# Kernel optimization log

Measured on AMD Instinct MI355X. Metric: run time of the kernel, lower is better.

## Reference

```python
import jax, jax.numpy as jnp
import numpy as np

B, SC, ST = 16, 512, 512
DP, DC = 256, 128
D = DP + 2 * DC          # 512 = d_model
H, L, DFF = 8, 2, 2048
NCAT, NCONT = 1000, 2048


def sin_embed(vals, d, scale=1000.0):
    # vectorized sinusoidal_time_embedding: even dims -> sin(angle), odd dims -> cos(angle)
    i = jnp.arange(d, dtype=jnp.float32)
    ang = vals.astype(jnp.float32)[..., None] / jnp.power(scale, i / d)
    return jnp.where(i % 2 == 0, jnp.sin(ang), jnp.cos(ang))


def layer_norm(x, g, b, eps=1e-5):
    m = jnp.mean(x, -1, keepdims=True)
    v = jnp.mean(jnp.square(x - m), -1, keepdims=True)
    return (x - m) / jnp.sqrt(v + eps) * g + b


def setup_inputs() -> dict:
    key = jax.random.key(0)
    ks = jax.random.split(key, 16)
    s = 0.02
    def n(k, shape, scale=s):
        return jax.random.normal(k, shape, dtype=jnp.float32) * scale
    return {
        "context_cat": jax.random.randint(ks[0], (B, SC), 0, NCAT),
        "context_time": jax.random.uniform(ks[1], (B, SC), dtype=jnp.float32) * 100.0,
        "context_f0": jax.random.uniform(ks[2], (B, SC), dtype=jnp.float32) * 500.0,
        "target_cat": jax.random.randint(ks[3], (B, ST), 0, NCAT),
        "target_time": jax.random.uniform(ks[4], (B, ST), dtype=jnp.float32) * 100.0,
        "target_f0": jax.random.uniform(ks[5], (B, ST), dtype=jnp.float32) * 500.0,
        "cat_table": n(ks[6], (NCAT, DP), 1.0),
        "cont_table": sin_embed(jnp.arange(NCONT, dtype=jnp.float32), DC),  # frozen sin table
        "pad_emb": n(ks[7], (D,), 1.0),
        "Wq": n(ks[8], (L, D, D)), "bq": jnp.zeros((L, D)),
        "Wk": n(ks[9], (L, D, D)), "bk": jnp.zeros((L, D)),
        "Wv": n(ks[10], (L, D, D)), "bv": jnp.zeros((L, D)),
        "Wo": n(ks[11], (L, D, D)), "bo": jnp.zeros((L, D)),
        "ln1g": jnp.ones((L, D)), "ln1b": jnp.zeros((L, D)),
        "ln2g": jnp.ones((L, D)), "ln2b": jnp.zeros((L, D)),
        "W1": n(ks[12], (L, D, DFF)), "b1": jnp.zeros((L, DFF)),
        "W2": n(ks[13], (L, DFF, D)), "b2": jnp.zeros((L, D)),
    }


def reference(context_cat, context_time, context_f0, target_cat, target_time, target_f0,
              cat_table, cont_table, pad_emb,
              Wq, bq, Wk, bk, Wv, bv, Wo, bo,
              ln1g, ln1b, ln2g, ln2b, W1, b1, W2, b2):
    def embed(cat, tm, f0):
        pad = cat < 0
        e = jnp.concatenate(
            [cat_table[jnp.maximum(cat, 0)], sin_embed(tm, DC), sin_embed(f0, DC)], axis=-1)
        return jnp.where(pad[..., None], pad_emb, e), pad

    ce, cp = embed(context_cat, context_time, context_f0)
    te, tp = embed(target_cat, target_time, target_f0)
    x = jnp.concatenate([ce, te], axis=1)                       # [B, SC+ST, D]
    bias = jnp.where(jnp.concatenate([cp, tp], 1), -1e9, 0.0)[:, None, None, :]
    hd = D // H
    inv_sqrt = 1.0 / np.sqrt(hd).astype(np.float32)

    def step(h, p):
        wq, bq_, wk, bk_, wv, bv_, wo, bo_, g1, c1, g2, c2, w1, d1, w2, d2 = p
        Bn, S, _ = h.shape
        q = (h @ wq + bq_).reshape(Bn, S, H, hd)
        k = (h @ wk + bk_).reshape(Bn, S, H, hd)
        v = (h @ wv + bv_).reshape(Bn, S, H, hd)
        scores = jnp.einsum('bqhd,bkhd->bhqk', q, k) * inv_sqrt + bias
        attn = jax.nn.softmax(scores, axis=-1)
        o = jnp.einsum('bhqk,bkhd->bqhd', attn, v).reshape(Bn, S, D)
        h = layer_norm(h + o @ wo + bo_, g1, c1)                # post-norm (torch default)
        f = jax.nn.relu(h @ w1 + d1) @ w2 + d2
        return layer_norm(h + f, g2, c2), None

    x, _ = jax.lax.scan(step, x, (Wq, bq, Wk, bk, Wv, bv, Wo, bo,
                                  ln1g, ln1b, ln2g, ln2b, W1, b1, W2, b2))
    out = x[:, SC:, :]
    pred_cat = out[..., :DP] @ cat_table.T
    pred_time = out[..., DP:DP + DC] @ cont_table.T
    pred_f0 = out[..., DP + DC:] @ cont_table.T
    return pred_cat, pred_time, pred_f0
```

## Files before the change

kernel.cpp:

```cpp
#include <hip/hip_runtime.h>


typedef _Float16 half8 __attribute__((ext_vector_type(8)));
typedef _Float16 half4 __attribute__((ext_vector_type(4)));
typedef float f32x4 __attribute__((ext_vector_type(4)));
typedef unsigned int uint2v __attribute__((ext_vector_type(2)));
typedef unsigned int uint4v __attribute__((ext_vector_type(4)));

__device__ __forceinline__ void gl2lds16(const _Float16* g, _Float16* l) {
    __builtin_amdgcn_global_load_lds(
        (const __attribute__((address_space(1))) void*)g,
        (__attribute__((address_space(3))) void*)l, 16, 0, 0);
}

__global__ void cast_f32_f16_k(const float* __restrict__ in, _Float16* __restrict__ out,
                               long nsrc, long ntot) {
    long i = (long)blockIdx.x * blockDim.x + threadIdx.x;
    long stride = (long)gridDim.x * blockDim.x;
    for (; i < ntot; i += stride) out[i] = i < nsrc ? (_Float16)in[i] : (_Float16)0.f;
}

__global__ void tcast_k(const float* __restrict__ in, _Float16* __restrict__ out,
                        int R, int C, long zs, int rowoff) {
    __shared__ float tile[32][33];
    long z = blockIdx.z;
    const float* src = in + z * (long)R * C;
    _Float16* dst = out + z * zs + (long)rowoff * R;
    int c0 = blockIdx.x * 32, r0 = blockIdx.y * 32;
    for (int i = threadIdx.y; i < 32; i += 8)
        tile[i][threadIdx.x] = src[(long)(r0 + i) * C + c0 + threadIdx.x];
    __syncthreads();
    for (int i = threadIdx.y; i < 32; i += 8)
        dst[(long)(c0 + i) * R + r0 + threadIdx.x] = (_Float16)tile[threadIdx.x][i];
}

__global__ void bcat_k(const float* __restrict__ bq, const float* __restrict__ bk,
                       const float* __restrict__ bv, float* __restrict__ out, int L) {
    int i = blockIdx.x * 256 + threadIdx.x;
    if (i >= L * 1536) return;
    int l = i / 1536, j = i - l * 1536;
    float v = j < 512 ? bq[l * 512 + j] : (j < 1024 ? bk[l * 512 + j - 512] : bv[l * 512 + j - 1024]);
    out[i] = v;
}

__global__ void vtrans_k(const _Float16* __restrict__ qkv, _Float16* __restrict__ vT) {
    __shared__ _Float16 tile[32][33];
    int bh = blockIdx.z; int b = bh >> 3, h = bh & 7;
    int s0 = blockIdx.x * 32, d0 = blockIdx.y * 32;
    const _Float16* src = qkv + ((long)b * 1024) * 1536 + 1024 + h * 64;
    _Float16* dst = vT + (long)bh * 64 * 1024;
    for (int i = threadIdx.y; i < 32; i += 8)
        tile[i][threadIdx.x] = src[(long)(s0 + i) * 1536 + d0 + threadIdx.x];
    __syncthreads();
    for (int i = threadIdx.y; i < 32; i += 8)
        dst[(long)(d0 + i) * 1024 + s0 + threadIdx.x] = tile[threadIdx.x][i];
}

__global__ __launch_bounds__(128) void embed_k(
    const int* __restrict__ ccat, const float* __restrict__ ctime, const float* __restrict__ cf0,
    const int* __restrict__ tcat, const float* __restrict__ ttime, const float* __restrict__ tf0,
    const float* __restrict__ cat_table, const float* __restrict__ pad_emb,
    float* __restrict__ xf, _Float16* __restrict__ xb, float* __restrict__ biasKey) {
    int t = blockIdx.x;
    int b = t >> 10, s = t & 1023;
    int j = b * 512 + (s & 511);
    int cat; float tm, f0;
    if (s < 512) { cat = ccat[j]; tm = ctime[j]; f0 = cf0[j]; }
    else         { cat = tcat[j]; tm = ttime[j]; f0 = tf0[j]; }
    bool pad = cat < 0;
    if (threadIdx.x == 0) biasKey[t] = pad ? -1e9f : 0.f;
    int c = cat < 0 ? 0 : cat;
    #pragma unroll
    for (int u = 0; u < 4; u++) {
        int d = threadIdx.x * 4 + u;
        float val;
        if (pad) val = pad_emb[d];
        else if (d < 256) val = cat_table[(long)c * 256 + d];
        else {
            float base = (d < 384) ? tm : f0;
            int i = (d < 384) ? (d - 256) : (d - 384);
            float ang = base / powf(1000.f, (float)i * (1.f / 128.f));
            val = (i & 1) ? cosf(ang) : sinf(ang);
        }
        long o = (long)t * 512 + d;
        xf[o] = val;
        xb[o] = (_Float16)val;
    }
}

__global__ __launch_bounds__(256) void layernorm_k(
    float* xf, _Float16* __restrict__ xb,
    const float* __restrict__ g, const float* __restrict__ beta) {
    long row = blockIdx.x;
    int tid = threadIdx.x;
    float* xr = xf + row * 512;
    float v0 = xr[tid], v1 = xr[tid + 256];
    float s = v0 + v1, q = v0 * v0 + v1 * v1;
    #pragma unroll
    for (int o = 32; o; o >>= 1) { s += __shfl_down(s, o); q += __shfl_down(q, o); }
    __shared__ float rs[4], rq[4];
    if ((tid & 63) == 0) { rs[tid >> 6] = s; rq[tid >> 6] = q; }
    __syncthreads();
    s = rs[0] + rs[1] + rs[2] + rs[3];
    q = rq[0] + rq[1] + rq[2] + rq[3];
    float mean = s * (1.f / 512.f);
    float var = q * (1.f / 512.f) - mean * mean;
    float rstd = rsqrtf(var + 1e-5f);
    float y0 = (v0 - mean) * rstd * g[tid] + beta[tid];
    float y1 = (v1 - mean) * rstd * g[tid + 256] + beta[tid + 256];
    xr[tid] = y0; xr[tid + 256] = y1;
    xb[row * 512 + tid] = (_Float16)y0;
    xb[row * 512 + tid + 256] = (_Float16)y1;
}

__global__ __launch_bounds__(512, 2) void flash_k(
    const _Float16* __restrict__ QKV, const _Float16* __restrict__ VT,
    const float* __restrict__ biasKey, _Float16* __restrict__ O) {
    const int S = 1024, D = 512, LDQ = 1536, NT = 16;
    int bh = blockIdx.x; int b = bh >> 3, h = bh & 7;
    int qt = blockIdx.y;
    int tid = threadIdx.x, w = tid >> 6, lane = tid & 63;
    int g = lane >> 4, q15 = lane & 15;

    __shared__ __align__(16) _Float16 Ks[2][64 * 64];
    __shared__ __align__(16) _Float16 VTs[2][64 * 64];
    __shared__ __align__(16) float biasLds[1024];

    {
        const float* bsrc = biasKey + (long)b * S;
        biasLds[tid]       = bsrc[tid] * 1.442695041f;
        biasLds[tid + 512] = bsrc[tid + 512] * 1.442695041f;
    }

    int qrow = qt * 128 + w * 16 + q15;
    const _Float16* qp = QKV + ((long)(b * S + qrow)) * LDQ + h * 64 + g * 8;
    half8 qf[2];
    qf[0] = *(const half8*)(qp);
    qf[1] = *(const half8*)(qp + 32);
    const _Float16 qsc = (_Float16)0.1803368801f;
    #pragma unroll
    for (int kk = 0; kk < 2; kk++)
        #pragma unroll
        for (int i = 0; i < 8; i++) qf[kk][i] *= qsc;

    const _Float16* kbase = QKV + 512 + ((long)b * S) * LDQ + h * 64;
    const _Float16* vbase = VT + (long)bh * 64 * S;

    auto stageK = [&](int buf, int kt) {
        int row = tid >> 3, p = tid & 7;
        int s = p ^ (row & 7);
        gl2lds16(kbase + (long)(kt * 64 + row) * LDQ + s * 8, &Ks[buf][tid * 8]);
    };
    auto stageV = [&](int buf, int kt) {
        int row = tid >> 3, p = tid & 7;
        int s = p ^ (row & 7);
        gl2lds16(vbase + (long)row * S + kt * 64 + s * 8, &VTs[buf][tid * 8]);
    };

    f32x4 acc_o[4];
    #pragma unroll
    for (int i = 0; i < 4; i++)
        #pragma unroll
        for (int r = 0; r < 4; r++) acc_o[i][r] = 0.f;
    float m_run = -1e30f, l_run = 0.f;
    bool gOdd = (g & 1) != 0;

    auto QK = [&](int kt, f32x4 (&s)[4]) {
        #pragma unroll
        for (int mf = 0; mf < 4; mf++)
            #pragma unroll
            for (int r = 0; r < 4; r++) s[mf][r] = 0.f;
        int buf = kt & 1;
        __builtin_amdgcn_s_setprio(1);
        #pragma unroll
        for (int kk = 0; kk < 2; kk++)
            #pragma unroll
            for (int mf = 0; mf < 4; mf++) {
                int row = mf * 16 + q15;
                half8 kf = *(const half8*)&Ks[buf][row * 64 + (((kk * 4 + g) ^ (row & 7)) * 8)];
                s[mf] = __builtin_amdgcn_mfma_f32_16x16x32_f16(kf, qf[kk], s[mf], 0, 0, 0);
            }
        __builtin_amdgcn_s_setprio(0);
    };

    auto SMPV = [&](int kt, f32x4 (&s)[4]) {
        float mt = -1e30f;
        #pragma unroll
        for (int mf = 0; mf < 4; mf++) {
            f32x4 b4 = *(const f32x4*)&biasLds[kt * 64 + mf * 16 + g * 4];
            #pragma unroll
            for (int r = 0; r < 4; r++) {
                float sv = s[mf][r] + b4[r];
                s[mf][r] = sv;
                mt = fmaxf(mt, sv);
            }
        }
        mt = fmaxf(mt, __shfl_xor(mt, 16));
        mt = fmaxf(mt, __shfl_xor(mt, 32));

        float rsum = 0.f;
        if (__all(mt - m_run <= 8.f)) {
            #pragma unroll
            for (int mf = 0; mf < 4; mf++)
                #pragma unroll
                for (int r = 0; r < 4; r++) {
                    float p = exp2f(s[mf][r] - m_run);
                    s[mf][r] = p; rsum += p;
                }
        } else {
            float m_new = fmaxf(m_run, mt);
            float scale = exp2f(m_run - m_new);
            #pragma unroll
            for (int mf = 0; mf < 4; mf++)
                #pragma unroll
                for (int r = 0; r < 4; r++) {
                    float p = exp2f(s[mf][r] - m_new);
                    s[mf][r] = p; rsum += p;
                }
            float sc[4];
            #pragma unroll
            for (int r = 0; r < 4; r++) sc[r] = __shfl(scale, g * 4 + r);
            #pragma unroll
            for (int nf = 0; nf < 4; nf++)
                #pragma unroll
                for (int r = 0; r < 4; r++) acc_o[nf][r] *= sc[r];
            l_run *= scale;
            m_run = m_new;
        }
        rsum += __shfl_xor(rsum, 16);
        rsum += __shfl_xor(rsum, 32);
        l_run += rsum;

        unsigned pk[4][2];
        #pragma unroll
        for (int mf = 0; mf < 4; mf++) {
            auto h0 = __builtin_amdgcn_cvt_pkrtz(s[mf][0], s[mf][1]);
            auto h1 = __builtin_amdgcn_cvt_pkrtz(s[mf][2], s[mf][3]);
            pk[mf][0] = __builtin_bit_cast(unsigned, h0);
            pk[mf][1] = __builtin_bit_cast(unsigned, h1);
        }

        int buf = kt & 1;
        #pragma unroll
        for (int kk = 0; kk < 2; kk++) {
            unsigned wA[2], wB[2];
            #pragma unroll
            for (int wi = 0; wi < 2; wi++) {
                uint2v r2 = __builtin_amdgcn_permlane32_swap(
                    pk[2 * kk][wi], pk[2 * kk + 1][wi], false, false);
                unsigned na = r2[0];
                unsigned nb = r2[1];
                unsigned sa = (unsigned)__builtin_amdgcn_ds_swizzle((int)na, 0x401F);
                unsigned sb = (unsigned)__builtin_amdgcn_ds_swizzle((int)nb, 0x401F);
                wA[wi] = gOdd ? sb : na;
                wB[wi] = gOdd ? nb : sa;
            }
            uint4v paw;
            paw[0] = wA[0]; paw[1] = wA[1]; paw[2] = wB[0]; paw[3] = wB[1];
            half8 pa = __builtin_bit_cast(half8, paw);
            __builtin_amdgcn_s_setprio(1);
            #pragma unroll
            for (int nf = 0; nf < 4; nf++) {
                int row = nf * 16 + q15;
                half8 vf = *(const half8*)&VTs[buf][row * 64 + (((kk * 4 + g) ^ (row & 7)) * 8)];
                acc_o[nf] = __builtin_amdgcn_mfma_f32_16x16x32_f16(pa, vf, acc_o[nf], 0, 0, 0);
            }
            __builtin_amdgcn_s_setprio(0);
        }
    };

    f32x4 sA[4], sB[4];
    stageK(0, 0); stageV(0, 0); stageK(1, 1);
    __syncthreads();
    QK(0, sA);

    for (int t = 0; t < NT; t += 2) {
        __syncthreads();
        if (t + 2 < NT) stageK(t & 1, t + 2);
        if (t + 1 < NT) stageV((t + 1) & 1, t + 1);
        if (t + 1 < NT) QK(t + 1, sB);
        SMPV(t, sA);
        __syncthreads();
        if (t + 3 < NT) stageK((t + 1) & 1, t + 3);
        if (t + 2 < NT) stageV(t & 1, t + 2);
        if (t + 2 < NT) QK(t + 2, sA);
        SMPV(t + 1, sB);
    }

    float linv = 1.f / l_run;
    float lv[4];
    #pragma unroll
    for (int r = 0; r < 4; r++) lv[r] = __shfl(linv, g * 4 + r);
    _Float16* obase = O + ((long)(b * S + qt * 128 + w * 16)) * D + h * 64;
    #pragma unroll
    for (int nf = 0; nf < 4; nf++)
        #pragma unroll
        for (int r = 0; r < 4; r++) {
            int row = g * 4 + r;
            obase[(long)row * D + nf * 16 + q15] = (_Float16)(acc_o[nf][r] * lv[r]);
        }
}

template<int NBUF>
__global__ __launch_bounds__(256) void gemm_nt(
    const _Float16* __restrict__ A, long lda, long sA1, long sA2,
    const _Float16* __restrict__ Bm, long ldb, long sB1, long sB2,
    float* Cf, _Float16* Cb, long ldc, long sC1, long sC2,
    const float* __restrict__ bias, long sb1, long sb2,
    const float* resid,
    int M, int N, int K, int Z2, float alpha, int relu) {
    int z = blockIdx.z;
    int z1 = z / Z2, z2 = z - z1 * Z2;
    A  += z1 * sA1 + z2 * sA2;
    Bm += z1 * sB1 + z2 * sB2;
    long coff = z1 * sC1 + z2 * sC2;
    if (bias) bias += z1 * sb1 + z2 * sb2;

    int gx = gridDim.x;
    int nwg = gx * gridDim.y;
    int bid = blockIdx.y * gx + blockIdx.x;
    int q = nwg >> 3, r = nwg & 7;
    int xcd = bid & 7, ii = bid >> 3;
    int swz = (xcd < r ? xcd * (q + 1) : r * (q + 1) + (xcd - r) * q) + ii;
    int m0 = (swz / gx) * 128;
    int n0 = (swz % gx) * 128;

    __shared__ __align__(16) _Float16 As[NBUF][128 * 32];
    __shared__ __align__(16) _Float16 Bs[NBUF][128 * 32];

    int tid = threadIdx.x;
    int lane = tid & 63;
    int w = tid >> 6;
    int wr = (w >> 1) << 6;
    int wc = (w & 1) << 6;

    f32x4 acc[4][4];
    #pragma unroll
    for (int i = 0; i < 4; i++)
        #pragma unroll
        for (int jj = 0; jj < 4; jj++) { acc[i][jj][0] = 0.f; acc[i][jj][1] = 0.f; acc[i][jj][2] = 0.f; acc[i][jj][3] = 0.f; }

    int fr = lane & 15;
    int g = lane >> 4;
    int rs8 = (g ^ (fr & 3)) * 8;

    auto stage = [&](int buf, int kt) {
        #pragma unroll
        for (int i = 0; i < 2; i++) {
            int idx = tid + i * 256;
            int row = idx >> 2, s = idx & 3;
            int sg = s ^ (row & 3);
            gl2lds16(A + (long)(m0 + row) * lda + kt * 32 + sg * 8, &As[buf][idx * 8]);
            gl2lds16(Bm + (long)(n0 + row) * ldb + kt * 32 + sg * 8, &Bs[buf][idx * 8]);
        }
    };

    auto compute = [&](int cur) {
        half8 af[4], bfv[4];
        #pragma unroll
        for (int m = 0; m < 4; m++) af[m] = *(const half8*)&As[cur][(wr + m * 16 + fr) * 32 + rs8];
        #pragma unroll
        for (int n = 0; n < 4; n++) bfv[n] = *(const half8*)&Bs[cur][(wc + n * 16 + fr) * 32 + rs8];
        #pragma unroll
        for (int m = 0; m < 4; m++)
            #pragma unroll
            for (int n = 0; n < 4; n++)
                acc[m][n] = __builtin_amdgcn_mfma_f32_16x16x32_f16(af[m], bfv[n], acc[m][n], 0, 0, 0);
    };

    int nk = K >> 5;
    if constexpr (NBUF == 2) {
        stage(0, 0);
        for (int t = 0; t < nk; ++t) {
            __builtin_amdgcn_s_barrier();
            if (t + 1 < nk) {
                stage((t + 1) & 1, t + 1);
                asm volatile("s_waitcnt vmcnt(4)" ::: "memory");
            } else {
                asm volatile("s_waitcnt vmcnt(0)" ::: "memory");
            }
            __builtin_amdgcn_s_barrier();
            __builtin_amdgcn_sched_barrier(0);
            compute(t & 1);
        }
    } else {
        stage(0, 0);
        stage(1, 1);
        for (int t = 0; t < nk; ++t) {
            if (t + 1 < nk) asm volatile("s_waitcnt vmcnt(4)" ::: "memory");
            else            asm volatile("s_waitcnt vmcnt(0)" ::: "memory");
            __builtin_amdgcn_s_barrier();
            __builtin_amdgcn_sched_barrier(0);
            if (t + 2 < nk) stage((t + 2) % 3, t + 2);
            compute(t % 3);
        }
    }

    int fq = lane >> 4;
    #pragma unroll
    for (int m = 0; m < 4; m++) {
        #pragma unroll
        for (int jj = 0; jj < 4; jj++) {
            long row = m0 + wr + m * 16 + fq * 4 + jj;
            #pragma unroll
            for (int n = 0; n < 4; n++) {
                int col = n0 + wc + n * 16 + fr;
                if (col < N) {
                    float v = acc[m][n][jj] * alpha;
                    if (bias) v += bias[col];
                    long o = coff + row * ldc + col;
                    if (resid) v += resid[o];
                    if (relu) v = fmaxf(v, 0.f);
                    if (Cf) Cf[o] = v;
                    if (Cb) Cb[o] = (_Float16)v;
                }
            }
        }
    }
}

extern "C" void kernel_launch(void* const* d_in, const int* in_sizes, int n_in,
                              void* d_out, int out_size, void* d_ws, size_t ws_size,
                              hipStream_t stream) {
    const int Bn = 16, S = 1024, D = 512, H = 8, L = 2, DFF = 2048, NCAT = 1000, NCONT = 2048;
    const long M = (long)Bn * S;

    const int*   ccat      = (const int*)d_in[0];
    const float* ctime     = (const float*)d_in[1];
    const float* cf0       = (const float*)d_in[2];
    const int*   tcat      = (const int*)d_in[3];
    const float* ttime     = (const float*)d_in[4];
    const float* tf0       = (const float*)d_in[5];
    const float* cat_table = (const float*)d_in[6];
    const float* cont_tab  = (const float*)d_in[7];
    const float* pad_emb   = (const float*)d_in[8];
    const float* Wq = (const float*)d_in[9];
    const float* bq = (const float*)d_in[10];
    const float* Wk = (const float*)d_in[11];
    const float* bk = (const float*)d_in[12];
    const float* Wv = (const float*)d_in[13];
    const float* bv = (const float*)d_in[14];
    const float* Wo = (const float*)d_in[15];
    const float* bo = (const float*)d_in[16];
    const float* ln1g = (const float*)d_in[17];
    const float* ln1b = (const float*)d_in[18];
    const float* ln2g = (const float*)d_in[19];
    const float* ln2b = (const float*)d_in[20];
    const float* W1 = (const float*)d_in[21];
    const float* b1 = (const float*)d_in[22];
    const float* W2 = (const float*)d_in[23];
    const float* b2 = (const float*)d_in[24];

    char* wsb = (char*)d_ws;
    size_t off = 0;
    auto alloc = [&](size_t bytes) -> void* {
        off = (off + 255) & ~(size_t)255;
        void* p = wsb + off; off += bytes; return p;
    };

    float*     xf      = (float*)alloc(M * D * 4);
    _Float16*  xb      = (_Float16*)alloc(M * D * 2);
    _Float16*  qkv     = (_Float16*)alloc(M * 3 * D * 2);
    _Float16*  vT      = (_Float16*)alloc(M * D * 2);
    _Float16*  ob      = (_Float16*)alloc(M * D * 2);
    float*     biasKey = (float*)alloc(M * 4);
    _Float16*  WqkvT = (_Float16*)alloc((size_t)L * 3 * D * D * 2);
    float*     bqkv  = (float*)alloc((size_t)L * 3 * D * 4);
    _Float16*  WoT  = (_Float16*)alloc((size_t)L * D * D * 2);
    _Float16*  W1T  = (_Float16*)alloc((size_t)L * D * DFF * 2);
    _Float16*  W2T  = (_Float16*)alloc((size_t)L * DFF * D * 2);
    _Float16*  catT = (_Float16*)alloc((size_t)1024 * 256 * 2);
    _Float16*  conT = (_Float16*)alloc((size_t)NCONT * 128 * 2);

    size_t need_ffh = (size_t)M * DFF * 2;
    _Float16* ffh;
    size_t offAl = (off + 255) & ~(size_t)255;
    if (offAl + need_ffh <= ws_size) ffh = (_Float16*)alloc(need_ffh);
    else ffh = (_Float16*)d_out;

    auto gemm = [&](const _Float16* A, long lda, long sA1, long sA2,
                    const _Float16* Bm, long ldb, long sB1, long sB2,
                    float* Cf, _Float16* Cb, long ldc, long sC1, long sC2,
                    const float* bias, long sb1, long sb2,
                    const float* resid, int Mm, int Nn, int Kk,
                    int Z1, int Z2, float alpha, int relu, int deep) {
        dim3 gdim((Nn + 127) / 128, (Mm + 127) / 128, Z1 * Z2);
        if (deep)
            gemm_nt<3><<<gdim, 256, 0, stream>>>(A, lda, sA1, sA2, Bm, ldb, sB1, sB2,
                                                 Cf, Cb, ldc, sC1, sC2, bias, sb1, sb2,
                                                 resid, Mm, Nn, Kk, Z2, alpha, relu);
        else
            gemm_nt<2><<<gdim, 256, 0, stream>>>(A, lda, sA1, sA2, Bm, ldb, sB1, sB2,
                                                 Cf, Cb, ldc, sC1, sC2, bias, sb1, sb2,
                                                 resid, Mm, Nn, Kk, Z2, alpha, relu);
    };

    dim3 tb(32, 8);
    tcast_k<<<dim3(D / 32, D / 32, L), tb, 0, stream>>>(Wq, WqkvT, D, D, (long)3 * D * D, 0);
    tcast_k<<<dim3(D / 32, D / 32, L), tb, 0, stream>>>(Wk, WqkvT, D, D, (long)3 * D * D, D);
    tcast_k<<<dim3(D / 32, D / 32, L), tb, 0, stream>>>(Wv, WqkvT, D, D, (long)3 * D * D, 2 * D);
    bcat_k<<<dim3((L * 1536 + 255) / 256), 256, 0, stream>>>(bq, bk, bv, bqkv, L);
    tcast_k<<<dim3(D / 32, D / 32, L), tb, 0, stream>>>(Wo, WoT, D, D, (long)D * D, 0);
    tcast_k<<<dim3(DFF / 32, D / 32, L), tb, 0, stream>>>(W1, W1T, D, DFF, (long)D * DFF, 0);
    tcast_k<<<dim3(D / 32, DFF / 32, L), tb, 0, stream>>>(W2, W2T, DFF, D, (long)DFF * D, 0);
    cast_f32_f16_k<<<dim3(512), 256, 0, stream>>>(cat_table, catT, (long)NCAT * 256, (long)1024 * 256);
    cast_f32_f16_k<<<dim3(512), 256, 0, stream>>>(cont_tab, conT, (long)NCONT * 128, (long)NCONT * 128);

    embed_k<<<dim3((unsigned)M), 128, 0, stream>>>(ccat, ctime, cf0, tcat, ttime, tf0,
                                                   cat_table, pad_emb, xf, xb, biasKey);

    for (int l = 0; l < L; l++) {
        gemm(xb, D, 0, 0, WqkvT + (size_t)l * 3 * D * D, D, 0, 0, nullptr, qkv, 3 * D, 0, 0,
             bqkv + (size_t)l * 3 * D, 0, 0, nullptr, (int)M, 3 * D, D, 1, 1, 1.f, 0, 0);
        vtrans_k<<<dim3(32, 2, Bn * H), tb, 0, stream>>>(qkv, vT);

        flash_k<<<dim3(Bn * H, S / 128), 512, 0, stream>>>(qkv, vT, biasKey, ob);

        gemm(ob, D, 0, 0, WoT + (size_t)l * D * D, D, 0, 0, xf, nullptr, D, 0, 0,
             bo + l * D, 0, 0, xf, (int)M, D, D, 1, 1, 1.f, 0, 1);
        layernorm_k<<<dim3((unsigned)M), 256, 0, stream>>>(xf, xb, ln1g + l * D, ln1b + l * D);

        gemm(xb, D, 0, 0, W1T + (size_t)l * D * DFF, D, 0, 0, nullptr, ffh, DFF, 0, 0,
             b1 + l * DFF, 0, 0, nullptr, (int)M, DFF, D, 1, 1, 1.f, 1, 0);
        gemm(ffh, DFF, 0, 0, W2T + (size_t)l * DFF * D, DFF, 0, 0, xf, nullptr, D, 0, 0,
             b2 + l * D, 0, 0, xf, (int)M, D, DFF, 1, 1, 1.f, 0, 1);
        layernorm_k<<<dim3((unsigned)M), 256, 0, stream>>>(xf, xb, ln2g + l * D, ln2b + l * D);
    }

    float* out_cat  = (float*)d_out;
    float* out_time = out_cat + (size_t)Bn * 512 * NCAT;
    float* out_f0   = out_time + (size_t)Bn * 512 * NCONT;
    gemm(xb + (size_t)512 * D, D, (long)S * D, 0,
         catT, 256, 0, 0,
         out_cat, nullptr, NCAT, (long)512 * NCAT, 0,
         nullptr, 0, 0, nullptr, 512, NCAT, 256, Bn, 1, 1.f, 0, 0);
    gemm(xb + (size_t)512 * D + 256, D, (long)S * D, 0,
         conT, 128, 0, 0,
         out_time, nullptr, NCONT, (long)512 * NCONT, 0,
         nullptr, 0, 0, nullptr, 512, NCONT, 128, Bn, 1, 1.f, 0, 0);
    gemm(xb + (size_t)512 * D + 384, D, (long)S * D, 0,
         conT, 128, 0, 0,
         out_f0, nullptr, NCONT, (long)512 * NCONT, 0,
         nullptr, 0, 0, nullptr, 512, NCONT, 128, Bn, 1, 1.f, 0, 0);
}
```

Measured before the change: 913.3 us.

## Keep residual stream in fp16 and merge time/f0 output GEMMs

Drops the fp32 residual copy. Embed, layernorm and the residual-add epilogues now read and write only fp16 buffers, using ping-pong buffers tb/hb. Layernorm switches to packed two-half loads and stores, and embed writes half4 vectors. The two cont-table output GEMMs are merged into one launch by using the z2 batch dimension. This cuts memory traffic and launches, but accumulating residuals in fp16 costs precision.

Measured after the change: 841.8 us. 1.08x faster.

```diff
diff --git a/kernel.cpp b/kernel.cpp
--- a/kernel.cpp
+++ b/kernel.cpp
@@ -60,7 +60,7 @@
     const int* __restrict__ ccat, const float* __restrict__ ctime, const float* __restrict__ cf0,
     const int* __restrict__ tcat, const float* __restrict__ ttime, const float* __restrict__ tf0,
     const float* __restrict__ cat_table, const float* __restrict__ pad_emb,
-    float* __restrict__ xf, _Float16* __restrict__ xb, float* __restrict__ biasKey) {
+    _Float16* __restrict__ xb, float* __restrict__ biasKey) {
     int t = blockIdx.x;
     int b = t >> 10, s = t & 1023;
     int j = b * 512 + (s & 511);
@@ -70,6 +70,7 @@
     bool pad = cat < 0;
     if (threadIdx.x == 0) biasKey[t] = pad ? -1e9f : 0.f;
     int c = cat < 0 ? 0 : cat;
+    half4 h4;
     #pragma unroll
     for (int u = 0; u < 4; u++) {
         int d = threadIdx.x * 4 + u;
@@ -82,19 +83,20 @@
             float ang = base / powf(1000.f, (float)i * (1.f / 128.f));
             val = (i & 1) ? cosf(ang) : sinf(ang);
         }
-        long o = (long)t * 512 + d;
-        xf[o] = val;
-        xb[o] = (_Float16)val;
+        h4[u] = (_Float16)val;
     }
+    *(half4*)&xb[(long)t * 512 + threadIdx.x * 4] = h4;
 }
 
 __global__ __launch_bounds__(256) void layernorm_k(
-    float* xf, _Float16* __restrict__ xb,
+    const _Float16* __restrict__ in, _Float16* __restrict__ out,
     const float* __restrict__ g, const float* __restrict__ beta) {
     long row = blockIdx.x;
     int tid = threadIdx.x;
-    float* xr = xf + row * 512;
-    float v0 = xr[tid], v1 = xr[tid + 256];
+    const unsigned* rw = (const unsigned*)(in + row * 512);
+    unsigned wo = rw[tid];
+    float v0 = (float)(_Float16)__builtin_bit_cast(_Float16, (unsigned short)(wo & 0xffff));
+    float v1 = (float)(_Float16)__builtin_bit_cast(_Float16, (unsigned short)(wo >> 16));
     float s = v0 + v1, q = v0 * v0 + v1 * v1;
     #pragma unroll
     for (int o = 32; o; o >>= 1) { s += __shfl_down(s, o); q += __shfl_down(q, o); }
@@ -106,11 +108,11 @@
     float mean = s * (1.f / 512.f);
     float var = q * (1.f / 512.f) - mean * mean;
     float rstd = rsqrtf(var + 1e-5f);
-    float y0 = (v0 - mean) * rstd * g[tid] + beta[tid];
-    float y1 = (v1 - mean) * rstd * g[tid + 256] + beta[tid + 256];
-    xr[tid] = y0; xr[tid + 256] = y1;
-    xb[row * 512 + tid] = (_Float16)y0;
-    xb[row * 512 + tid + 256] = (_Float16)y1;
+    float y0 = (v0 - mean) * rstd * g[tid * 2] + beta[tid * 2];
+    float y1 = (v1 - mean) * rstd * g[tid * 2 + 1] + beta[tid * 2 + 1];
+    unsigned short u0 = __builtin_bit_cast(unsigned short, (_Float16)y0);
+    unsigned short u1 = __builtin_bit_cast(unsigned short, (_Float16)y1);
+    ((unsigned*)(out + row * 512))[tid] = (unsigned)u0 | ((unsigned)u1 << 16);
 }
 
 __global__ __launch_bounds__(512, 2) void flash_k(
@@ -307,7 +309,7 @@
     const _Float16* __restrict__ Bm, long ldb, long sB1, long sB2,
     float* Cf, _Float16* Cb, long ldc, long sC1, long sC2,
     const float* __restrict__ bias, long sb1, long sb2,
-    const float* resid,
+    const _Float16* resid,
     int M, int N, int K, int Z2, float alpha, int relu) {
     int z = blockIdx.z;
     int z1 = z / Z2, z2 = z - z1 * Z2;
@@ -409,7 +411,7 @@
                     float v = acc[m][n][jj] * alpha;
                     if (bias) v += bias[col];
                     long o = coff + row * ldc + col;
-                    if (resid) v += resid[o];
+                    if (resid) v += (float)resid[o];
                     if (relu) v = fmaxf(v, 0.f);
                     if (Cf) Cf[o] = v;
                     if (Cb) Cb[o] = (_Float16)v;
@@ -458,8 +460,9 @@
         void* p = wsb + off; off += bytes; return p;
     };
 
-    float*     xf      = (float*)alloc(M * D * 4);
     _Float16*  xb      = (_Float16*)alloc(M * D * 2);
+    _Float16*  tb      = (_Float16*)alloc(M * D * 2);
+    _Float16*  hb      = (_Float16*)alloc(M * D * 2);
     _Float16*  qkv     = (_Float16*)alloc(M * 3 * D * 2);
     _Float16*  vT      = (_Float16*)alloc(M * D * 2);
     _Float16*  ob      = (_Float16*)alloc(M * D * 2);
@@ -482,7 +485,7 @@
                     const _Float16* Bm, long ldb, long sB1, long sB2,
                     float* Cf, _Float16* Cb, long ldc, long sC1, long sC2,
                     const float* bias, long sb1, long sb2,
-                    const float* resid, int Mm, int Nn, int Kk,
+                    const _Float16* resid, int Mm, int Nn, int Kk,
                     int Z1, int Z2, float alpha, int relu, int deep) {
         dim3 gdim((Nn + 127) / 128, (Mm + 127) / 128, Z1 * Z2);
         if (deep)
@@ -495,36 +498,36 @@
                                                  resid, Mm, Nn, Kk, Z2, alpha, relu);
     };
 
-    dim3 tb(32, 8);
-    tcast_k<<<dim3(D / 32, D / 32, L), tb, 0, stream>>>(Wq, WqkvT, D, D, (long)3 * D * D, 0);
-    tcast_k<<<dim3(D / 32, D / 32, L), tb, 0, stream>>>(Wk, WqkvT, D, D, (long)3 * D * D, D);
-    tcast_k<<<dim3(D / 32, D / 32, L), tb, 0, stream>>>(Wv, WqkvT, D, D, (long)3 * D * D, 2 * D);
+    dim3 tb8(32, 8);
+    tcast_k<<<dim3(D / 32, D / 32, L), tb8, 0, stream>>>(Wq, WqkvT, D, D, (long)3 * D * D, 0);
+    tcast_k<<<dim3(D / 32, D / 32, L), tb8, 0, stream>>>(Wk, WqkvT, D, D, (long)3 * D * D, D);
+    tcast_k<<<dim3(D / 32, D / 32, L), tb8, 0, stream>>>(Wv, WqkvT, D, D, (long)3 * D * D, 2 * D);
     bcat_k<<<dim3((L * 1536 + 255) / 256), 256, 0, stream>>>(bq, bk, bv, bqkv, L);
-    tcast_k<<<dim3(D / 32, D / 32, L), tb, 0, stream>>>(Wo, WoT, D, D, (long)D * D, 0);
-    tcast_k<<<dim3(DFF / 32, D / 32, L), tb, 0, stream>>>(W1, W1T, D, DFF, (long)D * DFF, 0);
-    tcast_k<<<dim3(D / 32, DFF / 32, L), tb, 0, stream>>>(W2, W2T, DFF, D, (long)DFF * D, 0);
+    tcast_k<<<dim3(D / 32, D / 32, L), tb8, 0, stream>>>(Wo, WoT, D, D, (long)D * D, 0);
+    tcast_k<<<dim3(DFF / 32, D / 32, L), tb8, 0, stream>>>(W1, W1T, D, DFF, (long)D * DFF, 0);
+    tcast_k<<<dim3(D / 32, DFF / 32, L), tb8, 0, stream>>>(W2, W2T, DFF, D, (long)DFF * D, 0);
     cast_f32_f16_k<<<dim3(512), 256, 0, stream>>>(cat_table, catT, (long)NCAT * 256, (long)1024 * 256);
     cast_f32_f16_k<<<dim3(512), 256, 0, stream>>>(cont_tab, conT, (long)NCONT * 128, (long)NCONT * 128);
 
     embed_k<<<dim3((unsigned)M), 128, 0, stream>>>(ccat, ctime, cf0, tcat, ttime, tf0,
-                                                   cat_table, pad_emb, xf, xb, biasKey);
+                                                   cat_table, pad_emb, xb, biasKey);
 
     for (int l = 0; l < L; l++) {
         gemm(xb, D, 0, 0, WqkvT + (size_t)l * 3 * D * D, D, 0, 0, nullptr, qkv, 3 * D, 0, 0,
              bqkv + (size_t)l * 3 * D, 0, 0, nullptr, (int)M, 3 * D, D, 1, 1, 1.f, 0, 0);
-        vtrans_k<<<dim3(32, 2, Bn * H), tb, 0, stream>>>(qkv, vT);
+        vtrans_k<<<dim3(32, 2, Bn * H), tb8, 0, stream>>>(qkv, vT);
 
         flash_k<<<dim3(Bn * H, S / 128), 512, 0, stream>>>(qkv, vT, biasKey, ob);
 
-        gemm(ob, D, 0, 0, WoT + (size_t)l * D * D, D, 0, 0, xf, nullptr, D, 0, 0,
-             bo + l * D, 0, 0, xf, (int)M, D, D, 1, 1, 1.f, 0, 1);
-        layernorm_k<<<dim3((unsigned)M), 256, 0, stream>>>(xf, xb, ln1g + l * D, ln1b + l * D);
-
-        gemm(xb, D, 0, 0, W1T + (size_t)l * D * DFF, D, 0, 0, nullptr, ffh, DFF, 0, 0,
+        gemm(ob, D, 0, 0, WoT + (size_t)l * D * D, D, 0, 0, nullptr, tb, D, 0, 0,
+             bo + l * D, 0, 0, xb, (int)M, D, D, 1, 1, 1.f, 0, 1);
+        layernorm_k<<<dim3((unsigned)M), 256, 0, stream>>>(tb, hb, ln1g + l * D, ln1b + l * D);
+
+        gemm(hb, D, 0, 0, W1T + (size_t)l * D * DFF, D, 0, 0, nullptr, ffh, DFF, 0, 0,
              b1 + l * DFF, 0, 0, nullptr, (int)M, DFF, D, 1, 1, 1.f, 1, 0);
-        gemm(ffh, DFF, 0, 0, W2T + (size_t)l * DFF * D, DFF, 0, 0, xf, nullptr, D, 0, 0,
-             b2 + l * D, 0, 0, xf, (int)M, D, DFF, 1, 1, 1.f, 0, 1);
-        layernorm_k<<<dim3((unsigned)M), 256, 0, stream>>>(xf, xb, ln2g + l * D, ln2b + l * D);
+        gemm(ffh, DFF, 0, 0, W2T + (size_t)l * DFF * D, DFF, 0, 0, nullptr, tb, D, 0, 0,
+             b2 + l * D, 0, 0, hb, (int)M, D, DFF, 1, 1, 1.f, 0, 1);
+        layernorm_k<<<dim3((unsigned)M), 256, 0, stream>>>(tb, xb, ln2g + l * D, ln2b + l * D);
     }
 
     float* out_cat  = (float*)d_out;
@@ -534,12 +537,8 @@
          catT, 256, 0, 0,
          out_cat, nullptr, NCAT, (long)512 * NCAT, 0,
          nullptr, 0, 0, nullptr, 512, NCAT, 256, Bn, 1, 1.f, 0, 0);
-    gemm(xb + (size_t)512 * D + 256, D, (long)S * D, 0,
+    gemm(xb + (size_t)512 * D + 256, D, (long)S * D, 128,
          conT, 128, 0, 0,
-         out_time, nullptr, NCONT, (long)512 * NCONT, 0,
-         nullptr, 0, 0, nullptr, 512, NCONT, 128, Bn, 1, 1.f, 0, 0);
-    gemm(xb + (size_t)512 * D + 384, D, (long)S * D, 0,
-         conT, 128, 0, 0,
-         out_f0, nullptr, NCONT, (long)512 * NCONT, 0,
-         nullptr, 0, 0, nullptr, 512, NCONT, 128, Bn, 1, 1.f, 0, 0);
-}
+         out_time, nullptr, NCONT, (long)512 * NCONT, (long)Bn * 512 * NCONT,
+         nullptr, 0, 0, nullptr, 512, NCONT, 128, Bn, 2, 1.f, 0, 0);
+}
```
